# Kernel tuning notes

Hardware: AMD Instinct MI355X
Metric: run time of the kernel (lower is better)

Reference implementation:

```python
import jax, jax.numpy as jnp
import numpy as np

B, G, D, E = 16, 2048, 2048, 32          # batch, genes, drug fp dim, gene embed dim
NL, NM, H, GS = 16, 4, 6, 64             # n leaves, n mids, term hidden, genes per leaf
GAMMA, NDRUG, EPS = 0.5, 1024, 1e-5

def _bn3(x):  # BatchNorm1d on [B, C, L], training stats, affine at init (gamma=1, beta=0)
    m = x.mean(axis=(0, 2), keepdims=True)
    v = x.var(axis=(0, 2), keepdims=True)
    return (x - m) / jnp.sqrt(v + EPS)

def _bn2(x):  # BatchNorm1d on [B, C]
    m = x.mean(axis=0, keepdims=True)
    v = x.var(axis=0, keepdims=True)
    return (x - m) / jnp.sqrt(v + EPS)

def _term(ci, W1, b1, Wc, bc, Wd, bd):
    # ci: [B, E, in] child input; returns ([B,H,E] 3d out, [B,H] 2d out)
    h = jnp.einsum('bei,hi->bhe', ci, W1) + b1[None, :, None]      # linear -> permute
    h = _bn3(h)
    c = jnp.einsum('bhe,kh->bke', h, Wc) + bc[None, :, None]       # context layer
    out3d = _bn3(c)                                                # [B,H,E]
    mean = out3d.mean(axis=1)                                      # [B,E]
    out2d = _bn2(jnp.tanh(mean @ Wd.T + bd))                       # dimension layer
    return out3d, out2d

def setup_inputs():
    key = jax.random.key(0)
    ks = iter(jax.random.split(key, 64))
    def rn(shape):
        return jax.random.normal(next(ks), shape, dtype=jnp.float32) * 0.05
    x = jax.random.normal(next(ks), (B, G + D + 1), dtype=jnp.float32)
    idx = jax.random.randint(next(ks), (B,), 0, NDRUG)
    x = x.at[:, -1].set(idx.astype(jnp.float32))
    table = jax.random.randint(next(ks), (NDRUG, G), 0, G, dtype=jnp.int32)
    inp = dict(x=x, table=table,
        W_rbf=rn((E, G)), b_rbf=rn((E,)), emb=rn((G, E)),
        W_dg=rn((NL, GS, G)), b_dg=rn((NL, GS)),
        Wl1=rn((NL, H, GS)), bl1=rn((NL, H)), Wlc=rn((NL, H, H)), blc=rn((NL, H)),
        Wld=rn((NL, H, E)), bld=rn((NL, H)),
        Wm1=rn((NM, H, 4 * H)), bm1=rn((NM, H)), Wmc=rn((NM, H, H)), bmc=rn((NM, H)),
        Wmd=rn((NM, H, E)), bmd=rn((NM, H)),
        Wr1=rn((H, 4 * H)), br1=rn((H,)), Wrc=rn((H, H)), brc=rn((H,)),
        Wrd=rn((H, E)), brd=rn((H,)),
        Wd1=rn((100, D)), bd1=rn((100,)), Wd2=rn((50, 100)), bd2=rn((50,)),
        Wd3=rn((H, 50)), bd3=rn((H,)),
        Wf=rn((6, 2 * H)), bf=rn((6,)), Wfa=rn((1, 6)), bfa=rn((1,)),
        Wfo=rn((1, 1)), bfo=rn((1,)))
    return inp

def reference(x, W_rbf, b_rbf, emb, W_dg, b_dg,
              Wl1, bl1, Wlc, blc, Wld, bld,
              Wm1, bm1, Wmc, bmc, Wmd, bmd,
              Wr1, br1, Wrc, brc, Wrd, brd,
              Wd1, bd1, Wd2, bd2, Wd3, bd3,
              Wf, bf, Wfa, bfa, Wfo, bfo, table):
    g = x[:, :G]
    drug = x[:, G:G + D]
    idx = x[:, G + D].astype(jnp.int32)
    # RBF kernel: [B, G, G]
    vect = jnp.exp(-GAMMA * jnp.square(g[:, :, None] - g[:, None, :]))
    gv = jnp.einsum('bij,ej->bie', vect, W_rbf) + b_rbf            # [B,G,E]
    lv = emb[table[idx]]                                            # [B,G,E]
    gf = (gv + lv).transpose(0, 2, 1)                               # [B,E,G]
    # per-leaf direct gene layers
    gene_out = jnp.einsum('beg,lkg->lbek', gf, W_dg) + b_dg[:, None, None, :]  # [NL,B,E,GS]
    leaf3d, _ = jax.vmap(_term)(gene_out, Wl1, bl1, Wlc, blc, Wld, bld)        # [NL,B,H,E]
    # mid terms: concat 4 leaf children along feature dim
    a = leaf3d.transpose(0, 1, 3, 2).reshape(NM, 4, B, E, H)
    a = jnp.moveaxis(a, 1, 3).reshape(NM, B, E, 4 * H)
    mid3d, _ = jax.vmap(_term)(a, Wm1, bm1, Wmc, bmc, Wmd, bmd)                # [NM,B,H,E]
    r = jnp.moveaxis(mid3d.transpose(0, 1, 3, 2), 0, 2).reshape(B, E, 4 * H)
    _, root2d = _term(r, Wr1, br1, Wrc, brc, Wrd, brd)                          # [B,H]
    # drug MLP
    d = drug
    for Wl, bl in ((Wd1, bd1), (Wd2, bd2), (Wd3, bd3)):
        d = _bn2(jnp.tanh(d @ Wl.T + bl))
    fin = jnp.concatenate([root2d, d], axis=1)                                  # [B,2H]
    out = _bn2(jnp.tanh(fin @ Wf.T + bf))
    aux = jnp.tanh(out @ Wfa.T + bfa)
    return aux @ Wfo.T + bfo                                                    # [B,1]
```

## Files before the change

### kernel.cpp

```cpp
#include <hip/hip_runtime.h>
#include <hip/hip_bf16.h>

#define Bb 16
#define Gg 2048
#define Dd 2048
#define XS 4097
#define EPSf 1e-5f
#define CEXP (-0.72134752044448170368f)

typedef unsigned int u32;
typedef __attribute__((ext_vector_type(8))) short bf16x8;
typedef __attribute__((ext_vector_type(4))) float f32x4;

union U16 { uint4 u; bf16x8 v; };

__device__ inline float fast_exp2(float x) {
#if __has_builtin(__builtin_amdgcn_exp2f)
  return __builtin_amdgcn_exp2f(x);
#else
  return exp2f(x);
#endif
}

__device__ inline u32 pk2(float a, float b) {
  return __builtin_amdgcn_perm(__float_as_uint(b), __float_as_uint(a), 0x07060302u);
}
__device__ inline float bftrunc(float a) {
  return __uint_as_float(__float_as_uint(a) & 0xFFFF0000u);
}

__device__ inline void split8(const float* f, U16& hi, U16& lo) {
  u32 h[4], l[4];
  #pragma unroll
  for (int p = 0; p < 4; ++p) {
    float a = f[2 * p], b = f[2 * p + 1];
    h[p] = pk2(a, b);
    l[p] = pk2(a - bftrunc(a), b - bftrunc(b));
  }
  hi.u = make_uint4(h[0], h[1], h[2], h[3]);
  lo.u = make_uint4(l[0], l[1], l[2], l[3]);
}

__device__ inline float wred(float v) {
  #pragma unroll
  for (int o = 32; o > 0; o >>= 1) v += __shfl_xor(v, o, 64);
  return v;
}

__global__ __launch_bounds__(256) void k_split(const float* __restrict__ Wrbf,
                                               const float* __restrict__ Wdg,
                                               u32* __restrict__ Rhi, u32* __restrict__ Rlo,
                                               u32* __restrict__ Dhi, u32* __restrict__ Dlo) {
  int c = blockIdx.x * 256 + threadIdx.x;
  const float* src;
  u32 *dhi, *dlo;
  if (c < 8192) {
    int h = c >> 12, ks = (c >> 6) & 63, l = c & 63;
    src = Wrbf + (h * 16 + (l & 15)) * Gg + ks * 32 + (l >> 4) * 8;
    dhi = Rhi + (size_t)c * 4; dlo = Rlo + (size_t)c * 4;
  } else {
    int cc = c - 8192;
    int nf = cc >> 12, ks = (cc >> 6) & 63, l = cc & 63;
    src = Wdg + (size_t)(nf * 16 + (l & 15)) * Gg + ks * 32 + (l >> 4) * 8;
    dhi = Dhi + (size_t)cc * 4; dlo = Dlo + (size_t)cc * 4;
  }
  float4 f0 = *(const float4*)src;
  float4 f1 = *(const float4*)(src + 4);
  float f[8] = {f0.x, f0.y, f0.z, f0.w, f1.x, f1.y, f1.z, f1.w};
  U16 hi, lo;
  split8(f, hi, lo);
  *(uint4*)dhi = hi.u;
  *(uint4*)dlo = lo.u;
}

__global__ __launch_bounds__(512) void k_rbf(const float* __restrict__ x,
                                             const u32* __restrict__ Whi,
                                             const u32* __restrict__ Wlo,
                                             const int* __restrict__ table,
                                             const float* __restrict__ emb,
                                             const float* __restrict__ brbf,
                                             u32* __restrict__ Ahi,
                                             u32* __restrict__ Alo) {
  __shared__ float g_s[2048];
  __shared__ u32 w_s[8192];
  const int tid = threadIdx.x;
  const int lane = tid & 63, wid = tid >> 6;
  const int b = blockIdx.y;
  const int i0w = blockIdx.x * 128 + wid * 16;
  #pragma unroll
  for (int q = 0; q < 4; ++q) g_s[tid * 4 + q] = x[(size_t)b * XS + tid * 4 + q];
  const float gi = x[(size_t)b * XS + i0w + (lane & 15)];
  f32x4 acc0 = {0.f, 0.f, 0.f, 0.f};
  f32x4 acc1 = {0.f, 0.f, 0.f, 0.f};
  const int jb = (lane >> 4) * 8;

  uint4 pf[4];
  #pragma unroll
  for (int sg = 0; sg < 4; ++sg) {
    int seg = wid * 4 + sg;
    int arr = seg >> 4, h = (seg >> 3) & 1, ksl = seg & 7;
    pf[sg] = *(const uint4*)((arr ? Wlo : Whi) +
             (((size_t)h * 64 + 0 * 8 + ksl) * 64 + lane) * 4);
  }
  for (int chunk = 0; chunk < 8; ++chunk) {
    __syncthreads();
    #pragma unroll
    for (int sg = 0; sg < 4; ++sg)
      *(uint4*)&w_s[(wid * 4 + sg) * 256 + lane * 4] = pf[sg];
    if (chunk < 7) {
      #pragma unroll
      for (int sg = 0; sg < 4; ++sg) {
        int seg = wid * 4 + sg;
        int arr = seg >> 4, h = (seg >> 3) & 1, ksl = seg & 7;
        pf[sg] = *(const uint4*)((arr ? Wlo : Whi) +
                 (((size_t)h * 64 + (chunk + 1) * 8 + ksl) * 64 + lane) * 4);
      }
    }
    __syncthreads();
    #pragma unroll
    for (int ksl = 0; ksl < 8; ++ksl) {
      const float* gp = &g_s[chunk * 256 + ksl * 32 + jb];
      float4 gja = *(const float4*)gp;
      float4 gjb = *(const float4*)(gp + 4);
      float gv[8] = {gja.x, gja.y, gja.z, gja.w, gjb.x, gjb.y, gjb.z, gjb.w};
      float kv[8];
      #pragma unroll
      for (int q = 0; q < 8; ++q) {
        float d = gi - gv[q];
        kv[q] = fast_exp2(d * d * CEXP);
      }
      U16 ah, al;
      split8(kv, ah, al);
      U16 w0h, w1h, w0l, w1l;
      w0h.u = *(const uint4*)&w_s[(ksl) * 256 + lane * 4];
      w1h.u = *(const uint4*)&w_s[(8 + ksl) * 256 + lane * 4];
      w0l.u = *(const uint4*)&w_s[(16 + ksl) * 256 + lane * 4];
      w1l.u = *(const uint4*)&w_s[(24 + ksl) * 256 + lane * 4];
      acc0 = __builtin_amdgcn_mfma_f32_16x16x32_bf16(ah.v, w0h.v, acc0, 0, 0, 0);
      acc0 = __builtin_amdgcn_mfma_f32_16x16x32_bf16(al.v, w0h.v, acc0, 0, 0, 0);
      acc0 = __builtin_amdgcn_mfma_f32_16x16x32_bf16(ah.v, w0l.v, acc0, 0, 0, 0);
      acc1 = __builtin_amdgcn_mfma_f32_16x16x32_bf16(ah.v, w1h.v, acc1, 0, 0, 0);
      acc1 = __builtin_amdgcn_mfma_f32_16x16x32_bf16(al.v, w1h.v, acc1, 0, 0, 0);
      acc1 = __builtin_amdgcn_mfma_f32_16x16x32_bf16(ah.v, w1l.v, acc1, 0, 0, 0);
    }
  }
  const int idx = (int)x[(size_t)b * XS + Gg + Dd];
  const int eloc = lane & 15, quad = lane >> 4;
  const int ks = i0w >> 5;
  const int lp = (2 * ((i0w >> 4) & 1) + (quad >> 1)) * 16 + eloc;
  const int hs = quad & 1;
  #pragma unroll
  for (int hb = 0; hb < 2; ++hb) {
    const int e = hb * 16 + eloc;
    const float bias = brbf[e];
    f32x4 a = hb ? acc1 : acc0;
    float v[4];
    #pragma unroll
    for (int r = 0; r < 4; ++r) {
      int i = i0w + quad * 4 + r;
      int t = table[idx * Gg + i];
      v[r] = a[r] + bias + emb[t * 32 + e];
    }
    size_t off = ((size_t)((b * 2 + hb) * 64 + ks) * 64 + lp) * 4 + hs * 2;
    Ahi[off]     = pk2(v[0], v[1]);
    Ahi[off + 1] = pk2(v[2], v[3]);
    Alo[off]     = pk2(v[0] - bftrunc(v[0]), v[1] - bftrunc(v[1]));
    Alo[off + 1] = pk2(v[2] - bftrunc(v[2]), v[3] - bftrunc(v[3]));
  }
}

__global__ __launch_bounds__(512) void k_mm(const u32* __restrict__ Ahi,
                                            const u32* __restrict__ Alo,
                                            const u32* __restrict__ Bhi,
                                            const u32* __restrict__ Blo,
                                            float* __restrict__ part) {
  __shared__ u32 s_mm[6144];
  const int tid = threadIdx.x;
  const int lane = tid & 63, wid = tid >> 6;
  const int id = blockIdx.x;
  const int pl = id & 7, by = (id >> 3) & 7, ph = id >> 6;
  const int p = ph * 8 + pl;
  const int bx = p >> 2, kc = p & 3;
  const int wm = wid >> 2, wn = wid & 3;
  f32x4 acc[2][2];
  #pragma unroll
  for (int mf = 0; mf < 2; ++mf)
    #pragma unroll
    for (int nf = 0; nf < 2; ++nf) acc[mf][nf] = (f32x4){0.f, 0.f, 0.f, 0.f};

  uint4 pf[3];
  #pragma unroll
  for (int q = 0; q < 3; ++q) {
    int seg = wid * 3 + q;
    const u32* src;
    if (seg < 8) {
      int hl = seg >> 2, mf = seg & 3;
      src = (hl ? Alo : Ahi) + (((size_t)(by * 4 + mf) * 64 + kc * 16) * 64 + lane) * 4;
    } else {
      int t = seg - 8, hl = t >> 3, nf = t & 7;
      src = (hl ? Blo : Bhi) + (((size_t)(bx * 8 + nf) * 64 + kc * 16) * 64 + lane) * 4;
    }
    pf[q] = *(const uint4*)src;
  }
  for (int stage = 0; stage < 16; ++stage) {
    __syncthreads();
    #pragma unroll
    for (int q = 0; q < 3; ++q)
      *(uint4*)&s_mm[(wid * 3 + q) * 256 + lane * 4] = pf[q];
    if (stage < 15) {
      const int ks = kc * 16 + stage + 1;
      #pragma unroll
      for (int q = 0; q < 3; ++q) {
        int seg = wid * 3 + q;
        const u32* src;
        if (seg < 8) {
          int hl = seg >> 2, mf = seg & 3;
          src = (hl ? Alo : Ahi) + (((size_t)(by * 4 + mf) * 64 + ks) * 64 + lane) * 4;
        } else {
          int t = seg - 8, hl = t >> 3, nf = t & 7;
          src = (hl ? Blo : Bhi) + (((size_t)(bx * 8 + nf) * 64 + ks) * 64 + lane) * 4;
        }
        pf[q] = *(const uint4*)src;
      }
    }
    __syncthreads();
    U16 ah[2], al[2], bh[2], bl[2];
    #pragma unroll
    for (int mf = 0; mf < 2; ++mf) {
      ah[mf].u = *(const uint4*)&s_mm[(0 + wm * 2 + mf) * 256 + lane * 4];
      al[mf].u = *(const uint4*)&s_mm[(4 + wm * 2 + mf) * 256 + lane * 4];
    }
    #pragma unroll
    for (int nf = 0; nf < 2; ++nf) {
      bh[nf].u = *(const uint4*)&s_mm[(8 + wn * 2 + nf) * 256 + lane * 4];
      bl[nf].u = *(const uint4*)&s_mm[(16 + wn * 2 + nf) * 256 + lane * 4];
    }
    #pragma unroll
    for (int mf = 0; mf < 2; ++mf) {
      #pragma unroll
      for (int nf = 0; nf < 2; ++nf) {
        acc[mf][nf] = __builtin_amdgcn_mfma_f32_16x16x32_bf16(ah[mf].v, bh[nf].v, acc[mf][nf], 0, 0, 0);
        acc[mf][nf] = __builtin_amdgcn_mfma_f32_16x16x32_bf16(al[mf].v, bh[nf].v, acc[mf][nf], 0, 0, 0);
        acc[mf][nf] = __builtin_amdgcn_mfma_f32_16x16x32_bf16(ah[mf].v, bl[nf].v, acc[mf][nf], 0, 0, 0);
      }
    }
  }
  const int quad = lane >> 4, nl = lane & 15;
  #pragma unroll
  for (int mf = 0; mf < 2; ++mf) {
    #pragma unroll
    for (int nf = 0; nf < 2; ++nf) {
      int n  = bx * 128 + wn * 32 + nf * 16 + nl;
      int m0 = by * 64 + wm * 32 + mf * 16 + quad * 4;
      float4 st = make_float4(acc[mf][nf][0], acc[mf][nf][1], acc[mf][nf][2], acc[mf][nf][3]);
      *(float4*)&part[(size_t)kc * 524288 + (size_t)n * 512 + m0] = st;
    }
  }
}

__global__ __launch_bounds__(256) void k_gout(const float4* __restrict__ part4,
                                              const float* __restrict__ bdg,
                                              float4* __restrict__ gout4) {
  int f4 = blockIdx.x * 256 + threadIdx.x;
  int n = f4 >> 7;
  float4 a = part4[f4];
  float4 b = part4[131072 + f4];
  float4 c = part4[262144 + f4];
  float4 d = part4[393216 + f4];
  float bias = bdg[n];
  gout4[f4] = make_float4(a.x + b.x + c.x + d.x + bias,
                          a.y + b.y + c.y + d.y + bias,
                          a.z + b.z + c.z + d.z + bias,
                          a.w + b.w + c.w + d.w + bias);
}

__device__ inline void bn512(float* v, int wv, int lane,
                             float (*r1)[6], float (*r2)[6]) {
  float s[6], q[6];
  #pragma unroll
  for (int c = 0; c < 6; ++c) {
    float a = v[c];
    s[c] = wred(a);
    q[c] = wred(a * a);
  }
  __syncthreads();
  if (lane == 0) {
    #pragma unroll
    for (int c = 0; c < 6; ++c) { r1[wv][c] = s[c]; r2[wv][c] = q[c]; }
  }
  __syncthreads();
  #pragma unroll
  for (int c = 0; c < 6; ++c) {
    float S = 0.f, Q = 0.f;
    #pragma unroll
    for (int w = 0; w < 8; ++w) { S += r1[w][c]; Q += r2[w][c]; }
    float m  = S * (1.0f / 512.0f);
    float va = Q * (1.0f / 512.0f) - m * m;
    v[c] = (v[c] - m) * rsqrtf(va + EPSf);
  }
}

__global__ __launch_bounds__(512) void k_leaf(const float* __restrict__ gout,
                                              const float* __restrict__ W1,
                                              const float* __restrict__ b1,
                                              const float* __restrict__ Wc,
                                              const float* __restrict__ bc,
                                              float* __restrict__ outp) {
  const int l = blockIdx.x, tid = threadIdx.x;
  const int wv = tid >> 6, lane = tid & 63;
  __shared__ float r1[8][6], r2[8][6];
  float cv[64];
  #pragma unroll
  for (int i = 0; i < 64; ++i)
    cv[i] = gout[(size_t)(l * 64 + i) * 512 + tid];
  const float* w1 = W1 + l * 6 * 64;
  float h[6];
  #pragma unroll
  for (int hh = 0; hh < 6; ++hh) {
    float s = b1[l * 6 + hh];
    #pragma unroll
    for (int i = 0; i < 64; ++i) s = fmaf(cv[i], w1[hh * 64 + i], s);
    h[hh] = s;
  }
  bn512(h, wv, lane, r1, r2);
  float c[6];
  #pragma unroll
  for (int k = 0; k < 6; ++k) {
    float s = bc[l * 6 + k];
    #pragma unroll
    for (int hh = 0; hh < 6; ++hh) s = fmaf(h[hh], Wc[l * 36 + k * 6 + hh], s);
    c[k] = s;
  }
  bn512(c, wv, lane, r1, r2);
  float* o = outp + (((size_t)(l >> 2) * 512 + tid) * 24 + (l & 3) * 6);
  #pragma unroll
  for (int k = 0; k < 6; ++k) o[k] = c[k];
}

__global__ __launch_bounds__(512) void k_mid(const float* __restrict__ gin,
                                             const float* __restrict__ W1,
                                             const float* __restrict__ b1,
                                             const float* __restrict__ Wc,
                                             const float* __restrict__ bc,
                                             float* __restrict__ outp) {
  const int l = blockIdx.x, tid = threadIdx.x;
  const int wv = tid >> 6, lane = tid & 63;
  __shared__ float r1[8][6], r2[8][6];
  const float* ci = gin + ((size_t)l * 512 + tid) * 24;
  float cv[24];
  #pragma unroll
  for (int q = 0; q < 6; ++q) *(float4*)&cv[q * 4] = ((const float4*)ci)[q];
  const float* w1 = W1 + l * 6 * 24;
  float h[6];
  #pragma unroll
  for (int hh = 0; hh < 6; ++hh) {
    float s = b1[l * 6 + hh];
    #pragma unroll
    for (int i = 0; i < 24; ++i) s = fmaf(cv[i], w1[hh * 24 + i], s);
    h[hh] = s;
  }
  bn512(h, wv, lane, r1, r2);
  float c[6];
  #pragma unroll
  for (int k = 0; k < 6; ++k) {
    float s = bc[l * 6 + k];
    #pragma unroll
    for (int hh = 0; hh < 6; ++hh) s = fmaf(h[hh], Wc[l * 36 + k * 6 + hh], s);
    c[k] = s;
  }
  bn512(c, wv, lane, r1, r2);
  float* o = outp + ((size_t)tid * 24 + l * 6);
  #pragma unroll
  for (int k = 0; k < 6; ++k) o[k] = c[k];
}

__global__ __launch_bounds__(512) void k_root(const float* __restrict__ rootin,
                                              const float* __restrict__ Wr1,
                                              const float* __restrict__ br1,
                                              const float* __restrict__ Wrc,
                                              const float* __restrict__ brc,
                                              const float* __restrict__ Wrd,
                                              const float* __restrict__ brd,
                                              float* __restrict__ r2d) {
  const int tid = threadIdx.x;
  const int wv = tid >> 6, lane = tid & 63;
  __shared__ float r1[8][6], r2[8][6];
  const float* ci = rootin + (size_t)tid * 24;
  float cv[24];
  #pragma unroll
  for (int q = 0; q < 6; ++q) *(float4*)&cv[q * 4] = ((const float4*)ci)[q];
  float h[6];
  #pragma unroll
  for (int hh = 0; hh < 6; ++hh) {
    float s = br1[hh];
    #pragma unroll
    for (int i = 0; i < 24; ++i) s = fmaf(cv[i], Wr1[hh * 24 + i], s);
    h[hh] = s;
  }
  bn512(h, wv, lane, r1, r2);
  float c[6];
  #pragma unroll
  for (int k = 0; k < 6; ++k) {
    float s = brc[k];
    #pragma unroll
    for (int hh = 0; hh < 6; ++hh) s = fmaf(h[hh], Wrc[k * 6 + hh], s);
    c[k] = s;
  }
  bn512(c, wv, lane, r1, r2);
  float mv = (c[0] + c[1] + c[2] + c[3] + c[4] + c[5]) * (1.0f / 6.0f);
  __shared__ float shm[512];
  shm[tid] = mv;
  __syncthreads();
  __shared__ float st[96];
  if (tid < 96) {
    int b = tid / 6, hh = tid % 6;
    float s = brd[hh];
    #pragma unroll
    for (int e = 0; e < 32; ++e) s = fmaf(shm[b * 32 + e], Wrd[hh * 32 + e], s);
    st[tid] = tanhf(s);
  }
  __syncthreads();
  if (tid < 6) {
    float S = 0.f, Q = 0.f;
    for (int b = 0; b < 16; ++b) { float v = st[b * 6 + tid]; S += v; Q += v * v; }
    float m = S * (1.0f / 16.0f), va = Q * (1.0f / 16.0f) - m * m;
    float iv = rsqrtf(va + EPSf);
    for (int b = 0; b < 16; ++b) r2d[b * 6 + tid] = (st[b * 6 + tid] - m) * iv;
  }
}

__global__ __launch_bounds__(1024) void k_drug1(const float* __restrict__ x,
                                                const float* __restrict__ Wd1,
                                                const float* __restrict__ bd1,
                                                float* __restrict__ d1) {
  const int c = blockIdx.x;
  const int tid = threadIdx.x;
  const int b = tid >> 6, lane = tid & 63;
  const float* xb = x + (size_t)b * XS + Gg;
  const float* w = Wd1 + (size_t)c * 2048;
  float s = 0.f;
  #pragma unroll
  for (int q = 0; q < 8; ++q) {
    int k = q * 256 + lane * 4;
    float4 xv = *(const float4*)(xb + k);
    float4 wv = *(const float4*)(w + k);
    s = fmaf(xv.x, wv.x, s);
    s = fmaf(xv.y, wv.y, s);
    s = fmaf(xv.z, wv.z, s);
    s = fmaf(xv.w, wv.w, s);
  }
  s = wred(s);
  __shared__ float y[16];
  if (lane == 0) y[b] = tanhf(s + bd1[c]);
  __syncthreads();
  if (tid < 16) {
    float S = 0.f, Q = 0.f;
    #pragma unroll
    for (int bb = 0; bb < 16; ++bb) { float v = y[bb]; S += v; Q += v * v; }
    float m = S * (1.0f / 16.0f), va = Q * (1.0f / 16.0f) - m * m;
    d1[tid * 100 + c] = (y[tid] - m) * rsqrtf(va + EPSf);
  }
}

__global__ __launch_bounds__(512) void k_final(const float* __restrict__ d1,
                                               const float* __restrict__ r2d,
                                               const float* __restrict__ Wd2,
                                               const float* __restrict__ bd2,
                                               const float* __restrict__ Wd3,
                                               const float* __restrict__ bd3,
                                               const float* __restrict__ Wf,
                                               const float* __restrict__ bf,
                                               const float* __restrict__ Wfa,
                                               const float* __restrict__ bfa,
                                               const float* __restrict__ Wfo,
                                               const float* __restrict__ bfo,
                                               float* __restrict__ out) {
  const int tid = threadIdx.x;
  __shared__ float w2s[50 * 101];
  __shared__ float d1s[1600];
  for (int u = tid; u < 5000; u += 512) w2s[(u / 100) * 101 + (u % 100)] = Wd2[u];
  for (int u = tid; u < 1600; u += 512) d1s[u] = d1[u];
  __syncthreads();
  __shared__ float s2[800], mu2[50], iv2[50];
  for (int u = tid; u < 800; u += 512) {
    int b = u / 50, c = u % 50;
    float s = bd2[c];
    #pragma unroll
    for (int k = 0; k < 100; ++k) s = fmaf(d1s[b * 100 + k], w2s[c * 101 + k], s);
    s2[u] = tanhf(s);
  }
  __syncthreads();
  if (tid < 50) {
    float S = 0.f, Q = 0.f;
    #pragma unroll
    for (int b = 0; b < 16; ++b) { float v = s2[b * 50 + tid]; S += v; Q += v * v; }
    float m = S * (1.0f / 16.0f), va = Q * (1.0f / 16.0f) - m * m;
    mu2[tid] = m; iv2[tid] = rsqrtf(va + EPSf);
  }
  __syncthreads();
  __shared__ float s3[96], mu3[6], iv3[6];
  if (tid < 96) {
    int b = tid / 6, c = tid % 6;
    float s = bd3[c];
    #pragma unroll
    for (int k = 0; k < 50; ++k)
      s = fmaf((s2[b * 50 + k] - mu2[k]) * iv2[k], Wd3[c * 50 + k], s);
    s3[tid] = tanhf(s);
  }
  __syncthreads();
  if (tid < 6) {
    float S = 0.f, Q = 0.f;
    #pragma unroll
    for (int b = 0; b < 16; ++b) { float v = s3[b * 6 + tid]; S += v; Q += v * v; }
    float m = S * (1.0f / 16.0f), va = Q * (1.0f / 16.0f) - m * m;
    mu3[tid] = m; iv3[tid] = rsqrtf(va + EPSf);
  }
  __syncthreads();
  __shared__ float sf[96], muf[6], ivf[6];
  if (tid < 96) {
    int b = tid / 6, c = tid % 6;
    float s = bf[c];
    #pragma unroll
    for (int q = 0; q < 6; ++q) s = fmaf(r2d[b * 6 + q], Wf[c * 12 + q], s);
    #pragma unroll
    for (int q = 0; q < 6; ++q)
      s = fmaf((s3[b * 6 + q] - mu3[q]) * iv3[q], Wf[c * 12 + 6 + q], s);
    sf[tid] = tanhf(s);
  }
  __syncthreads();
  if (tid < 6) {
    float S = 0.f, Q = 0.f;
    #pragma unroll
    for (int b = 0; b < 16; ++b) { float v = sf[b * 6 + tid]; S += v; Q += v * v; }
    float m = S * (1.0f / 16.0f), va = Q * (1.0f / 16.0f) - m * m;
    muf[tid] = m; ivf[tid] = rsqrtf(va + EPSf);
  }
  __syncthreads();
  if (tid < 16) {
    float s = bfa[0];
    #pragma unroll
    for (int q = 0; q < 6; ++q)
      s = fmaf((sf[tid * 6 + q] - muf[q]) * ivf[q], Wfa[q], s);
    float a = tanhf(s);
    out[tid] = a * Wfo[0] + bfo[0];
  }
}

extern "C" void kernel_launch(void* const* d_in, const int* in_sizes, int n_in,
                              void* d_out, int out_size, void* d_ws, size_t ws_size,
                              hipStream_t stream) {
  const float* x     = (const float*)d_in[0];
  const int*   table = (const int*)d_in[1];
  const float* Wrbf  = (const float*)d_in[2];
  const float* brbf  = (const float*)d_in[3];
  const float* emb   = (const float*)d_in[4];
  const float* Wdg   = (const float*)d_in[5];
  const float* bdg   = (const float*)d_in[6];
  const float* Wl1   = (const float*)d_in[7];
  const float* bl1   = (const float*)d_in[8];
  const float* Wlc   = (const float*)d_in[9];
  const float* blc   = (const float*)d_in[10];
  const float* Wm1   = (const float*)d_in[13];
  const float* bm1   = (const float*)d_in[14];
  const float* Wmc   = (const float*)d_in[15];
  const float* bmc   = (const float*)d_in[16];
  const float* Wr1   = (const float*)d_in[19];
  const float* br1   = (const float*)d_in[20];
  const float* Wrc   = (const float*)d_in[21];
  const float* brc   = (const float*)d_in[22];
  const float* Wrd   = (const float*)d_in[23];
  const float* brd   = (const float*)d_in[24];
  const float* Wd1   = (const float*)d_in[25];
  const float* bd1   = (const float*)d_in[26];
  const float* Wd2   = (const float*)d_in[27];
  const float* bd2   = (const float*)d_in[28];
  const float* Wd3   = (const float*)d_in[29];
  const float* bd3   = (const float*)d_in[30];
  const float* Wf    = (const float*)d_in[31];
  const float* bf    = (const float*)d_in[32];
  const float* Wfa   = (const float*)d_in[33];
  const float* bfa   = (const float*)d_in[34];
  const float* Wfo   = (const float*)d_in[35];
  const float* bfo   = (const float*)d_in[36];
  float* out = (float*)d_out;

  u32* Rhi = (u32*)d_ws;
  u32* Rlo = Rhi + 32768;
  u32* Dhi = Rlo + 32768;
  u32* Dlo = Dhi + 1048576;
  u32* Ahi = Dlo + 1048576;
  u32* Alo = Ahi + 524288;
  float* partB = (float*)(Alo + 524288);
  float* gout  = partB + 4 * 524288;
  float* midin = gout + 524288;
  float* rootin= midin + 49152;
  float* r2d   = rootin + 12288;
  float* d1    = r2d + 96;

  hipLaunchKernelGGL(k_drug1, dim3(100),    dim3(1024), 0, stream, x, Wd1, bd1, d1);
  hipLaunchKernelGGL(k_split, dim3(1056),   dim3(256),  0, stream, Wrbf, Wdg, Rhi, Rlo, Dhi, Dlo);
  hipLaunchKernelGGL(k_rbf,   dim3(16, 16), dim3(512),  0, stream, x, Rhi, Rlo, table, emb, brbf, Ahi, Alo);
  hipLaunchKernelGGL(k_mm,    dim3(256),    dim3(512),  0, stream, Ahi, Alo, Dhi, Dlo, partB);
  hipLaunchKernelGGL(k_gout,  dim3(512),    dim3(256),  0, stream, (const float4*)partB, bdg, (float4*)gout);
  hipLaunchKernelGGL(k_leaf,  dim3(16),     dim3(512),  0, stream, gout, Wl1, bl1, Wlc, blc, midin);
  hipLaunchKernelGGL(k_mid,   dim3(4),      dim3(512),  0, stream, midin, Wm1, bm1, Wmc, bmc, rootin);
  hipLaunchKernelGGL(k_root,  dim3(1),      dim3(512),  0, stream, rootin, Wr1, br1, Wrc, brc, Wrd, brd, r2d);
  hipLaunchKernelGGL(k_final, dim3(1),      dim3(512),  0, stream, d1, r2d, Wd2, bd2, Wd3, bd3,
                     Wf, bf, Wfa, bfa, Wfo, bfo, out);
}
```

Baseline: 128.7 us.

## Split RBF kernel over K into four chunks with separate reduce-and-pack kernel

The RBF projection kernel now splits the 2048-long gene reduction into four chunks across a new grid dimension, going from 256 to 1024 blocks. Each block writes fp32 partial accumulators to a workspace buffer. A new k_pack kernel sums the four partials, adds the bias and the embedding lookup, and writes the bf16 hi/lo packed layout. This raises parallelism in the exp/MFMA-heavy stage, at the cost of an extra launch and a 16 MB partial-sum round trip through memory.

```diff
diff --git a/kernel.cpp b/kernel.cpp
--- a/kernel.cpp
+++ b/kernel.cpp
@@ -76,23 +76,19 @@
 __global__ __launch_bounds__(512) void k_rbf(const float* __restrict__ x,
                                              const u32* __restrict__ Whi,
                                              const u32* __restrict__ Wlo,
-                                             const int* __restrict__ table,
-                                             const float* __restrict__ emb,
-                                             const float* __restrict__ brbf,
-                                             u32* __restrict__ Ahi,
-                                             u32* __restrict__ Alo) {
-  __shared__ float g_s[2048];
+                                             float4* __restrict__ partR) {
+  __shared__ float g_s[512];
   __shared__ u32 w_s[8192];
   const int tid = threadIdx.x;
   const int lane = tid & 63, wid = tid >> 6;
-  const int b = blockIdx.y;
-  const int i0w = blockIdx.x * 128 + wid * 16;
-  #pragma unroll
-  for (int q = 0; q < 4; ++q) g_s[tid * 4 + q] = x[(size_t)b * XS + tid * 4 + q];
+  const int it = blockIdx.x, b = blockIdx.y, jc = blockIdx.z;
+  const int i0w = it * 128 + wid * 16;
+  g_s[tid] = x[(size_t)b * XS + jc * 512 + tid];
   const float gi = x[(size_t)b * XS + i0w + (lane & 15)];
   f32x4 acc0 = {0.f, 0.f, 0.f, 0.f};
   f32x4 acc1 = {0.f, 0.f, 0.f, 0.f};
   const int jb = (lane >> 4) * 8;
+  const int ksbase = jc * 16;
 
   uint4 pf[4];
   #pragma unroll
@@ -100,20 +96,20 @@
     int seg = wid * 4 + sg;
     int arr = seg >> 4, h = (seg >> 3) & 1, ksl = seg & 7;
     pf[sg] = *(const uint4*)((arr ? Wlo : Whi) +
-             (((size_t)h * 64 + 0 * 8 + ksl) * 64 + lane) * 4);
-  }
-  for (int chunk = 0; chunk < 8; ++chunk) {
+             (((size_t)h * 64 + ksbase + ksl) * 64 + lane) * 4);
+  }
+  for (int chunk = 0; chunk < 2; ++chunk) {
     __syncthreads();
     #pragma unroll
     for (int sg = 0; sg < 4; ++sg)
       *(uint4*)&w_s[(wid * 4 + sg) * 256 + lane * 4] = pf[sg];
-    if (chunk < 7) {
+    if (chunk < 1) {
       #pragma unroll
       for (int sg = 0; sg < 4; ++sg) {
         int seg = wid * 4 + sg;
         int arr = seg >> 4, h = (seg >> 3) & 1, ksl = seg & 7;
         pf[sg] = *(const uint4*)((arr ? Wlo : Whi) +
-                 (((size_t)h * 64 + (chunk + 1) * 8 + ksl) * 64 + lane) * 4);
+                 (((size_t)h * 64 + ksbase + 8 + ksl) * 64 + lane) * 4);
       }
     }
     __syncthreads();
@@ -144,29 +140,44 @@
       acc1 = __builtin_amdgcn_mfma_f32_16x16x32_bf16(ah.v, w1l.v, acc1, 0, 0, 0);
     }
   }
-  const int idx = (int)x[(size_t)b * XS + Gg + Dd];
-  const int eloc = lane & 15, quad = lane >> 4;
-  const int ks = i0w >> 5;
-  const int lp = (2 * ((i0w >> 4) & 1) + (quad >> 1)) * 16 + eloc;
-  const int hs = quad & 1;
-  #pragma unroll
-  for (int hb = 0; hb < 2; ++hb) {
-    const int e = hb * 16 + eloc;
-    const float bias = brbf[e];
-    f32x4 a = hb ? acc1 : acc0;
-    float v[4];
-    #pragma unroll
-    for (int r = 0; r < 4; ++r) {
-      int i = i0w + quad * 4 + r;
-      int t = table[idx * Gg + i];
-      v[r] = a[r] + bias + emb[t * 32 + e];
-    }
-    size_t off = ((size_t)((b * 2 + hb) * 64 + ks) * 64 + lp) * 4 + hs * 2;
-    Ahi[off]     = pk2(v[0], v[1]);
-    Ahi[off + 1] = pk2(v[2], v[3]);
-    Alo[off]     = pk2(v[0] - bftrunc(v[0]), v[1] - bftrunc(v[1]));
-    Alo[off + 1] = pk2(v[2] - bftrunc(v[2]), v[3] - bftrunc(v[3]));
-  }
+  size_t pbase = (((((size_t)jc * 16 + b) * 16 + it) * 8 + wid) * 2) * 64 + lane;
+  partR[pbase]      = make_float4(acc0[0], acc0[1], acc0[2], acc0[3]);
+  partR[pbase + 64] = make_float4(acc1[0], acc1[1], acc1[2], acc1[3]);
+}
+
+__global__ __launch_bounds__(256) void k_pack(const float4* __restrict__ partR,
+                                              const float* __restrict__ x,
+                                              const int* __restrict__ table,
+                                              const float* __restrict__ emb,
+                                              const float* __restrict__ brbf,
+                                              u32* __restrict__ Ahi,
+                                              u32* __restrict__ Alo) {
+  int u = blockIdx.x * 256 + threadIdx.x;
+  int lane = u & 63, hb = (u >> 6) & 1, wid = (u >> 7) & 7;
+  int it = (u >> 10) & 15, b = u >> 14;
+  float4 p0 = partR[u];
+  float4 p1 = partR[262144 + u];
+  float4 p2 = partR[524288 + u];
+  float4 p3 = partR[786432 + u];
+  int eloc = lane & 15, quad = lane >> 4;
+  int e = hb * 16 + eloc;
+  int i0w = it * 128 + wid * 16;
+  int ib = i0w + quad * 4;
+  int idx = (int)x[(size_t)b * XS + Gg + Dd];
+  int4 tt = *(const int4*)&table[(size_t)idx * Gg + ib];
+  float bias = brbf[e];
+  float v0 = p0.x + p1.x + p2.x + p3.x + bias + emb[tt.x * 32 + e];
+  float v1 = p0.y + p1.y + p2.y + p3.y + bias + emb[tt.y * 32 + e];
+  float v2 = p0.z + p1.z + p2.z + p3.z + bias + emb[tt.z * 32 + e];
+  float v3 = p0.w + p1.w + p2.w + p3.w + bias + emb[tt.w * 32 + e];
+  int ks = i0w >> 5;
+  int lp = (2 * ((i0w >> 4) & 1) + (quad >> 1)) * 16 + eloc;
+  int hs = quad & 1;
+  size_t off = (((size_t)(b * 2 + hb) * 64 + ks) * 64 + lp) * 4 + hs * 2;
+  Ahi[off]     = pk2(v0, v1);
+  Ahi[off + 1] = pk2(v2, v3);
+  Alo[off]     = pk2(v0 - bftrunc(v0), v1 - bftrunc(v1));
+  Alo[off + 1] = pk2(v2 - bftrunc(v2), v3 - bftrunc(v3));
 }
 
 __global__ __launch_bounds__(512) void k_mm(const u32* __restrict__ Ahi,
@@ -590,21 +601,23 @@
   u32* Dlo = Dhi + 1048576;
   u32* Ahi = Dlo + 1048576;
   u32* Alo = Ahi + 524288;
-  float* partB = (float*)(Alo + 524288);
+  float4* partR = (float4*)(Alo + 524288);
+  float* partB = (float*)(partR + 1048576);
   float* gout  = partB + 4 * 524288;
   float* midin = gout + 524288;
   float* rootin= midin + 49152;
   float* r2d   = rootin + 12288;
   float* d1    = r2d + 96;
 
-  hipLaunchKernelGGL(k_drug1, dim3(100),    dim3(1024), 0, stream, x, Wd1, bd1, d1);
-  hipLaunchKernelGGL(k_split, dim3(1056),   dim3(256),  0, stream, Wrbf, Wdg, Rhi, Rlo, Dhi, Dlo);
-  hipLaunchKernelGGL(k_rbf,   dim3(16, 16), dim3(512),  0, stream, x, Rhi, Rlo, table, emb, brbf, Ahi, Alo);
-  hipLaunchKernelGGL(k_mm,    dim3(256),    dim3(512),  0, stream, Ahi, Alo, Dhi, Dlo, partB);
-  hipLaunchKernelGGL(k_gout,  dim3(512),    dim3(256),  0, stream, (const float4*)partB, bdg, (float4*)gout);
-  hipLaunchKernelGGL(k_leaf,  dim3(16),     dim3(512),  0, stream, gout, Wl1, bl1, Wlc, blc, midin);
-  hipLaunchKernelGGL(k_mid,   dim3(4),      dim3(512),  0, stream, midin, Wm1, bm1, Wmc, bmc, rootin);
-  hipLaunchKernelGGL(k_root,  dim3(1),      dim3(512),  0, stream, rootin, Wr1, br1, Wrc, brc, Wrd, brd, r2d);
-  hipLaunchKernelGGL(k_final, dim3(1),      dim3(512),  0, stream, d1, r2d, Wd2, bd2, Wd3, bd3,
+  hipLaunchKernelGGL(k_drug1, dim3(100),       dim3(1024), 0, stream, x, Wd1, bd1, d1);
+  hipLaunchKernelGGL(k_split, dim3(1056),      dim3(256),  0, stream, Wrbf, Wdg, Rhi, Rlo, Dhi, Dlo);
+  hipLaunchKernelGGL(k_rbf,   dim3(16, 16, 4), dim3(512),  0, stream, x, Rhi, Rlo, partR);
+  hipLaunchKernelGGL(k_pack,  dim3(1024),      dim3(256),  0, stream, partR, x, table, emb, brbf, Ahi, Alo);
+  hipLaunchKernelGGL(k_mm,    dim3(256),       dim3(512),  0, stream, Ahi, Alo, Dhi, Dlo, partB);
+  hipLaunchKernelGGL(k_gout,  dim3(512),       dim3(256),  0, stream, (const float4*)partB, bdg, (float4*)gout);
+  hipLaunchKernelGGL(k_leaf,  dim3(16),        dim3(512),  0, stream, gout, Wl1, bl1, Wlc, blc, midin);
+  hipLaunchKernelGGL(k_mid,   dim3(4),         dim3(512),  0, stream, midin, Wm1, bm1, Wmc, bmc, rootin);
+  hipLaunchKernelGGL(k_root,  dim3(1),         dim3(512),  0, stream, rootin, Wr1, br1, Wrc, brc, Wrd, brd, r2d);
+  hipLaunchKernelGGL(k_final, dim3(1),         dim3(512),  0, stream, d1, r2d, Wd2, bd2, Wd3, bd3,
                      Wf, bf, Wfa, bfa, Wfo, bfo, out);
 }
```

Result: no change. 126.2 us (-1.9%).
